# Kernel tuning notes

Measured on AMD Instinct MI355X. Metric: run time of the kernel, lower is better.

## Reference

```python
import jax, jax.numpy as jnp
import numpy as np

N_NODES = 50000


def gcn_conv(h, src, dst, W, b, n):
    # PyG GCNConv: x' = D^{-1/2} (A + I) D^{-1/2} (h W) + b
    x = h @ W  # [N, out]
    deg = jax.ops.segment_sum(jnp.ones_like(src, dtype=x.dtype), dst, num_segments=n) + 1.0  # self-loop
    dis = deg ** -0.5
    norm = dis[src] * dis[dst]  # [E]
    msg = x[src] * norm[:, None]  # [E, out]
    agg = jax.ops.segment_sum(msg, dst, num_segments=n)
    agg = agg + x * (dis * dis)[:, None]  # self-loop term: 1/deg_i * x_i
    return agg + b


def setup_inputs() -> dict:
    key = jax.random.key(0)
    ks = jax.random.split(key, 8)
    n, e = N_NODES, 800000
    d_in, d_rni, h = 128, 32, 256
    x = jax.random.normal(ks[0], (n, d_in), dtype=jnp.float32)
    rni = jax.random.normal(ks[1], (n, d_rni), dtype=jnp.float32)
    edge_index = jax.random.randint(ks[2], (2, e), 0, n, dtype=jnp.int64)
    s1 = (d_in + d_rni) ** -0.5
    s2 = h ** -0.5
    W1 = jax.random.normal(ks[3], (d_in + d_rni, h), dtype=jnp.float32) * s1
    b1 = jnp.zeros((h,), dtype=jnp.float32)
    W2 = jax.random.normal(ks[4], (h, h), dtype=jnp.float32) * s2
    b2 = jnp.zeros((h,), dtype=jnp.float32)
    W_out = jax.random.normal(ks[5], (h, h), dtype=jnp.float32) * s2
    b_out = jnp.zeros((h,), dtype=jnp.float32)
    return {"x": x, "rni": rni, "edge_index": edge_index, "W1": W1, "b1": b1,
            "W2": W2, "b2": b2, "W_out": W_out, "b_out": b_out}


def reference(x, rni, edge_index, W1, b1, W2, b2, W_out, b_out):
    n = x.shape[0]
    src, dst = edge_index[0], edge_index[1]
    h = jnp.concatenate([x, rni], axis=-1)  # RNI concat
    h = jax.nn.relu(gcn_conv(h, src, dst, W1, b1, n))
    h = jax.nn.relu(gcn_conv(h, src, dst, W2, b2, n))
    return h @ W_out + b_out
```

## Files before the change

kernel.cpp:

```cpp
#include <hip/hip_runtime.h>
#include <hip/hip_bf16.h>
#include <hip/hip_fp16.h>
#include <math.h>

#define D_IN   128
#define D_RNI  32
#define HID    256

typedef _Float16 half8 __attribute__((ext_vector_type(8)));
typedef float    f32x4 __attribute__((ext_vector_type(4)));

__global__ void k_detect(const unsigned int* __restrict__ w, int nwords, int* __restrict__ mode) {
    __shared__ unsigned int red[256];
    unsigned int acc = 0;
    for (int i = threadIdx.x; i < 1024; i += 256) {
        int idx = 2 * i + 1;
        if (idx < nwords) acc |= w[idx];
    }
    red[threadIdx.x] = acc;
    __syncthreads();
    for (int s = 128; s > 0; s >>= 1) {
        if (threadIdx.x < s) red[threadIdx.x] |= red[threadIdx.x + s];
        __syncthreads();
    }
    if (threadIdx.x == 0) *mode = (red[0] == 0u) ? 1 : 0;
}

__global__ void k_count(const unsigned int* __restrict__ ew, const int* __restrict__ mode_p,
                        int* __restrict__ counts, int e) {
    int mode = *mode_p;
    int i = blockIdx.x * 256 + threadIdx.x;
    if (i >= e) return;
    int d = mode ? (int)ew[2 * ((size_t)e + i)] : (int)ew[(size_t)e + i];
    atomicAdd(&counts[d], 1);
}

__global__ __launch_bounds__(1024) void k_scan1(const int* __restrict__ counts,
                                                int* __restrict__ incl,
                                                int* __restrict__ bsum, int n) {
    __shared__ int sd[1024];
    int t = threadIdx.x;
    int i = blockIdx.x * 1024 + t;
    int v = (i < n) ? counts[i] : 0;
    sd[t] = v;
    __syncthreads();
    for (int off = 1; off < 1024; off <<= 1) {
        int tmp = (t >= off) ? sd[t - off] : 0;
        __syncthreads();
        sd[t] += tmp;
        __syncthreads();
    }
    if (i < n) incl[i] = sd[t];
    if (t == 1023) bsum[blockIdx.x] = sd[1023];
}

__global__ __launch_bounds__(1024) void k_scan2(int* __restrict__ bsum, int nb) {
    __shared__ int sd[1024];
    int t = threadIdx.x;
    int v = (t < nb) ? bsum[t] : 0;
    sd[t] = v;
    __syncthreads();
    for (int off = 1; off < 1024; off <<= 1) {
        int tmp = (t >= off) ? sd[t - off] : 0;
        __syncthreads();
        sd[t] += tmp;
        __syncthreads();
    }
    if (t < nb) bsum[t] = sd[t] - v;
    if (t == nb - 1) bsum[nb] = sd[t];
}

__global__ void k_scan3(const int* __restrict__ counts, const int* __restrict__ incl,
                        const int* __restrict__ bsum,
                        int* __restrict__ rowptr, int* __restrict__ cursor,
                        float* __restrict__ dis, int n, int nb) {
    int i = blockIdx.x * 256 + threadIdx.x;
    if (i >= n) return;
    int excl = incl[i] - counts[i] + bsum[i >> 10];
    rowptr[i] = excl;
    cursor[i] = excl;
    dis[i] = 1.0f / sqrtf((float)(counts[i] + 1));
    if (i == 0) rowptr[n] = bsum[nb];
}

__global__ void k_scatter(const unsigned int* __restrict__ ew, const int* __restrict__ mode_p,
                          int* __restrict__ cursor, int* __restrict__ csr, int e) {
    int mode = *mode_p;
    int i = blockIdx.x * 256 + threadIdx.x;
    if (i >= e) return;
    int s, d;
    if (mode) {
        s = (int)ew[2 * (size_t)i];
        d = (int)ew[2 * ((size_t)e + i)];
    } else {
        s = (int)ew[(size_t)i];
        d = (int)ew[(size_t)e + i];
    }
    int pos = atomicAdd(&cursor[d], 1);
    csr[pos] = s;
}

__global__ void k_cvt_wt(const float* __restrict__ W, __half* __restrict__ Wt,
                         int K, int N, int total) {
    int i = blockIdx.x * 256 + threadIdx.x;
    if (i >= total) return;
    int k = i / N, nn = i - k * N;
    Wt[(size_t)nn * K + k] = __float2half(W[i]);
}

#define KT 32
#define LSTR 40
template <bool A_F32, bool ADD_BIAS, bool HALF_OUT>
__global__ __launch_bounds__(256) void k_mgemm(const void* __restrict__ Av, int strideA, int KA,
                                               const void* __restrict__ A2v, int strideA2,
                                               const __half* __restrict__ Bt,
                                               const float* __restrict__ bias,
                                               void* Cv, int M, int K) {
    __shared__ __half As[64 * LSTR];
    __shared__ __half Bs[256 * LSTR];
    int tid = threadIdx.x;
    int wave = tid >> 6, lane = tid & 63;
    int q = lane >> 4, m16 = lane & 15;
    int r0 = blockIdx.x * 64;

    f32x4 acc[4][4] = {};

    for (int k0 = 0; k0 < K; k0 += KT) {
        __syncthreads();
        {
            int r = tid >> 2, kq = (tid & 3) * 8;
            int row = r0 + r; if (row >= M) row = M - 1;
            if (A_F32) {
                const float* src; int stride, kk0;
                if (k0 < KA) { src = (const float*)Av;  stride = strideA;  kk0 = k0; }
                else         { src = (const float*)A2v; stride = strideA2; kk0 = k0 - KA; }
                const float* p = &src[(size_t)row * stride + kk0 + kq];
                float4 va = *reinterpret_cast<const float4*>(p);
                float4 vb = *reinterpret_cast<const float4*>(p + 4);
                union { __half2 h2[4]; uint4 u; } uu;
                uu.h2[0] = __floats2half2_rn(va.x, va.y);
                uu.h2[1] = __floats2half2_rn(va.z, va.w);
                uu.h2[2] = __floats2half2_rn(vb.x, vb.y);
                uu.h2[3] = __floats2half2_rn(vb.z, vb.w);
                *reinterpret_cast<uint4*>(&As[r * LSTR + kq]) = uu.u;
            } else {
                const __half* src = (const __half*)Av;
                uint4 v = *reinterpret_cast<const uint4*>(&src[(size_t)row * strideA + k0 + kq]);
                *reinterpret_cast<uint4*>(&As[r * LSTR + kq]) = v;
            }
        }
        {
            int nb = tid >> 2, kq = (tid & 3) * 8;
            #pragma unroll
            for (int i = 0; i < 4; ++i) {
                int nn = nb + i * 64;
                uint4 v = *reinterpret_cast<const uint4*>(&Bt[(size_t)nn * K + k0 + kq]);
                *reinterpret_cast<uint4*>(&Bs[nn * LSTR + kq]) = v;
            }
        }
        __syncthreads();

        half8 af[4], bf[4];
        #pragma unroll
        for (int mi = 0; mi < 4; ++mi)
            af[mi] = *reinterpret_cast<const half8*>(&As[(mi * 16 + m16) * LSTR + q * 8]);
        #pragma unroll
        for (int ni = 0; ni < 4; ++ni)
            bf[ni] = *reinterpret_cast<const half8*>(&Bs[(wave * 64 + ni * 16 + m16) * LSTR + q * 8]);
        #pragma unroll
        for (int mi = 0; mi < 4; ++mi)
            #pragma unroll
            for (int ni = 0; ni < 4; ++ni)
                acc[mi][ni] = __builtin_amdgcn_mfma_f32_16x16x32_f16(af[mi], bf[ni], acc[mi][ni], 0, 0, 0);
    }

    #pragma unroll
    for (int mi = 0; mi < 4; ++mi) {
        #pragma unroll
        for (int r = 0; r < 4; ++r) {
            int row = r0 + mi * 16 + q * 4 + r;
            if (row >= M) continue;
            #pragma unroll
            for (int ni = 0; ni < 4; ++ni) {
                int col = wave * 64 + ni * 16 + m16;
                float v = acc[mi][ni][r];
                if (ADD_BIAS) v += bias[col];
                if (HALF_OUT) ((__half*)Cv)[(size_t)row * HID + col] = __float2half(v);
                else          ((float*)Cv)[(size_t)row * HID + col] = v;
            }
        }
    }
}

__global__ __launch_bounds__(256) void k_agg(const __half* __restrict__ xh,
                                             const int* __restrict__ rowptr,
                                             const int* __restrict__ csr,
                                             const float* __restrict__ dis,
                                             const float* __restrict__ bias,
                                             __half* __restrict__ outh, int n) {
    int i = blockIdx.x * 4 + (threadIdx.x >> 6);
    if (i >= n) return;
    int lane = threadIdx.x & 63;
    int c4 = lane * 4;
    float disd = dis[i];
    int e0 = rowptr[i], e1 = rowptr[i + 1];

    float acc0, acc1, acc2, acc3;
    {
        uint2 v = *reinterpret_cast<const uint2*>(&xh[(size_t)i * HID + c4]);
        float2 f0 = __half22float2(*reinterpret_cast<__half2*>(&v.x));
        float2 f1 = __half22float2(*reinterpret_cast<__half2*>(&v.y));
        float ws = disd * disd;
        acc0 = f0.x * ws; acc1 = f0.y * ws; acc2 = f1.x * ws; acc3 = f1.y * ws;
    }

    for (int e = e0; e < e1; e += 64) {
        int cnt = min(64, e1 - e);
        int sreg = 0; float wreg = 0.0f;
        if (lane < cnt) {
            sreg = csr[e + lane];
            wreg = dis[sreg] * disd;
        }
        int j = 0;
        for (; j + 4 <= cnt; j += 4) {
            int   s0 = __shfl(sreg, j + 0), s1 = __shfl(sreg, j + 1);
            int   s2 = __shfl(sreg, j + 2), s3 = __shfl(sreg, j + 3);
            float w0 = __shfl(wreg, j + 0), w1 = __shfl(wreg, j + 1);
            float w2 = __shfl(wreg, j + 2), w3 = __shfl(wreg, j + 3);
            uint2 v0 = *reinterpret_cast<const uint2*>(&xh[(size_t)s0 * HID + c4]);
            uint2 v1 = *reinterpret_cast<const uint2*>(&xh[(size_t)s1 * HID + c4]);
            uint2 v2 = *reinterpret_cast<const uint2*>(&xh[(size_t)s2 * HID + c4]);
            uint2 v3 = *reinterpret_cast<const uint2*>(&xh[(size_t)s3 * HID + c4]);
            float2 a0 = __half22float2(*reinterpret_cast<__half2*>(&v0.x));
            float2 b0 = __half22float2(*reinterpret_cast<__half2*>(&v0.y));
            float2 a1 = __half22float2(*reinterpret_cast<__half2*>(&v1.x));
            float2 b1 = __half22float2(*reinterpret_cast<__half2*>(&v1.y));
            float2 a2 = __half22float2(*reinterpret_cast<__half2*>(&v2.x));
            float2 b2 = __half22float2(*reinterpret_cast<__half2*>(&v2.y));
            float2 a3 = __half22float2(*reinterpret_cast<__half2*>(&v3.x));
            float2 b3 = __half22float2(*reinterpret_cast<__half2*>(&v3.y));
            acc0 = fmaf(a0.x, w0, acc0); acc1 = fmaf(a0.y, w0, acc1);
            acc2 = fmaf(b0.x, w0, acc2); acc3 = fmaf(b0.y, w0, acc3);
            acc0 = fmaf(a1.x, w1, acc0); acc1 = fmaf(a1.y, w1, acc1);
            acc2 = fmaf(b1.x, w1, acc2); acc3 = fmaf(b1.y, w1, acc3);
            acc0 = fmaf(a2.x, w2, acc0); acc1 = fmaf(a2.y, w2, acc1);
            acc2 = fmaf(b2.x, w2, acc2); acc3 = fmaf(b2.y, w2, acc3);
            acc0 = fmaf(a3.x, w3, acc0); acc1 = fmaf(a3.y, w3, acc1);
            acc2 = fmaf(b3.x, w3, acc2); acc3 = fmaf(b3.y, w3, acc3);
        }
        for (; j < cnt; ++j) {
            int   s = __shfl(sreg, j);
            float w = __shfl(wreg, j);
            uint2 v = *reinterpret_cast<const uint2*>(&xh[(size_t)s * HID + c4]);
            float2 a = __half22float2(*reinterpret_cast<__half2*>(&v.x));
            float2 b = __half22float2(*reinterpret_cast<__half2*>(&v.y));
            acc0 = fmaf(a.x, w, acc0); acc1 = fmaf(a.y, w, acc1);
            acc2 = fmaf(b.x, w, acc2); acc3 = fmaf(b.y, w, acc3);
        }
    }

    float4 bb = *reinterpret_cast<const float4*>(&bias[c4]);
    union { __half2 h2[2]; uint2 u; } o;
    o.h2[0] = __floats2half2_rn(fmaxf(acc0 + bb.x, 0.0f), fmaxf(acc1 + bb.y, 0.0f));
    o.h2[1] = __floats2half2_rn(fmaxf(acc2 + bb.z, 0.0f), fmaxf(acc3 + bb.w, 0.0f));
    *reinterpret_cast<uint2*>(&outh[(size_t)i * HID + c4]) = o.u;
}

extern "C" void kernel_launch(void* const* d_in, const int* in_sizes, int n_in,
                              void* d_out, int out_size, void* d_ws, size_t ws_size,
                              hipStream_t stream) {
    const float* x     = (const float*)d_in[0];
    const float* rni   = (const float*)d_in[1];
    const unsigned int* ew = (const unsigned int*)d_in[2];
    const float* W1    = (const float*)d_in[3];
    const float* b1    = (const float*)d_in[4];
    const float* W2    = (const float*)d_in[5];
    const float* b2    = (const float*)d_in[6];
    const float* W_out = (const float*)d_in[7];
    const float* b_out = (const float*)d_in[8];
    float* out = (float*)d_out;

    const int n  = in_sizes[0] / D_IN;
    const int e  = in_sizes[2] / 2;
    const int nb = (n + 1023) / 1024;
    const int K1 = D_IN + D_RNI;

    char* ws = (char*)d_ws;
    size_t off = 0;
    auto carve = [&](size_t bytes) {
        char* p = ws + off;
        off = (off + bytes + 255) & ~(size_t)255;
        return p;
    };
    __half* xh    = (__half*)carve((size_t)n * HID * sizeof(__half));
    __half* h     = (__half*)carve((size_t)n * HID * sizeof(__half));
    __half* W1t   = (__half*)carve((size_t)K1 * HID * sizeof(__half));
    __half* W2t   = (__half*)carve((size_t)HID * HID * sizeof(__half));
    __half* Wot   = (__half*)carve((size_t)HID * HID * sizeof(__half));
    int*   counts = (int*)carve((size_t)n * sizeof(int));
    int*   incl   = (int*)carve((size_t)n * sizeof(int));
    int*   bsum   = (int*)carve((size_t)(nb + 1) * sizeof(int));
    int*   rowptr = (int*)carve((size_t)(n + 1) * sizeof(int));
    int*   cursor = (int*)carve((size_t)n * sizeof(int));
    float* dis    = (float*)carve((size_t)n * sizeof(float));
    int*   csr    = (int*)carve((size_t)e * sizeof(int));
    int*   mode   = (int*)carve(sizeof(int));
    (void)ws_size;

    const int eb = (e + 255) / 256;
    const int gemm_blocks = (n + 63) / 64;
    const int agg_blocks  = (n + 3) / 4;

    k_detect<<<1, 256, 0, stream>>>(ew, 2 * e, mode);
    hipMemsetAsync(counts, 0, (size_t)n * sizeof(int), stream);
    k_count<<<eb, 256, 0, stream>>>(ew, mode, counts, e);
    k_scan1<<<nb, 1024, 0, stream>>>(counts, incl, bsum, n);
    k_scan2<<<1, 1024, 0, stream>>>(bsum, nb);
    k_scan3<<<(n + 255) / 256, 256, 0, stream>>>(counts, incl, bsum, rowptr, cursor, dis, n, nb);
    k_scatter<<<eb, 256, 0, stream>>>(ew, mode, cursor, csr, e);

    {
        int tw1 = K1 * HID;
        k_cvt_wt<<<(tw1 + 255) / 256, 256, 0, stream>>>(W1, W1t, K1, HID, tw1);
        int tw = HID * HID;
        k_cvt_wt<<<(tw + 255) / 256, 256, 0, stream>>>(W2, W2t, HID, HID, tw);
        k_cvt_wt<<<(tw + 255) / 256, 256, 0, stream>>>(W_out, Wot, HID, HID, tw);
    }

    k_mgemm<true, false, true><<<gemm_blocks, 256, 0, stream>>>(x, D_IN, D_IN, rni, D_RNI,
                                                                W1t, nullptr, xh, n, K1);
    k_agg<<<agg_blocks, 256, 0, stream>>>(xh, rowptr, csr, dis, b1, h, n);

    k_mgemm<false, false, true><<<gemm_blocks, 256, 0, stream>>>(h, HID, HID, nullptr, 0,
                                                                 W2t, nullptr, xh, n, HID);
    k_agg<<<agg_blocks, 256, 0, stream>>>(xh, rowptr, csr, dis, b2, h, n);

    k_mgemm<false, true, false><<<gemm_blocks, 256, 0, stream>>>(h, HID, HID, nullptr, 0,
                                                                 Wot, b_out, out, n, HID);
}
```

Measured before the change: 390.4 us.

## Chunk feature layout into column slabs and precompute edge weights in CSR

The GEMM's half-precision output is now written in a column-chunked layout: 8 slabs of 32 columns, each contiguous per node. Aggregation blocks each handle one slab, so the gathered working set per pass is smaller and cache-friendlier. The scatter kernel stores (src, normalized weight) pairs, which removes the per-edge dis lookup during aggregation. Each wave processes 8 edges in parallel and reduces them with shuffles. This doubles CSR storage and adds a cross-lane reduction per node, in exchange for better L2 locality of the gathers.

```diff
diff --git a/kernel.cpp b/kernel.cpp
--- a/kernel.cpp
+++ b/kernel.cpp
@@ -6,6 +6,7 @@
 #define D_IN   128
 #define D_RNI  32
 #define HID    256
+#define NCHUNK 8
 
 typedef _Float16 half8 __attribute__((ext_vector_type(8)));
 typedef float    f32x4 __attribute__((ext_vector_type(4)));
@@ -84,7 +85,8 @@
 }
 
 __global__ void k_scatter(const unsigned int* __restrict__ ew, const int* __restrict__ mode_p,
-                          int* __restrict__ cursor, int* __restrict__ csr, int e) {
+                          int* __restrict__ cursor, const float* __restrict__ dis,
+                          uint2* __restrict__ csrw, int e) {
     int mode = *mode_p;
     int i = blockIdx.x * 256 + threadIdx.x;
     if (i >= e) return;
@@ -96,8 +98,12 @@
         s = (int)ew[(size_t)i];
         d = (int)ew[(size_t)e + i];
     }
+    float w = dis[s] * dis[d];
     int pos = atomicAdd(&cursor[d], 1);
-    csr[pos] = s;
+    uint2 m;
+    m.x = (unsigned int)s;
+    m.y = __float_as_uint(w);
+    csrw[pos] = m;
 }
 
 __global__ void k_cvt_wt(const float* __restrict__ W, __half* __restrict__ Wt,
@@ -185,8 +191,12 @@
                 int col = wave * 64 + ni * 16 + m16;
                 float v = acc[mi][ni][r];
                 if (ADD_BIAS) v += bias[col];
-                if (HALF_OUT) ((__half*)Cv)[(size_t)row * HID + col] = __float2half(v);
-                else          ((float*)Cv)[(size_t)row * HID + col] = v;
+                if (HALF_OUT) {
+                    size_t addr = ((size_t)(col >> 5) * M + row) * 32 + (col & 31);
+                    ((__half*)Cv)[addr] = __float2half(v);
+                } else {
+                    ((float*)Cv)[(size_t)row * HID + col] = v;
+                }
             }
         }
     }
@@ -194,76 +204,61 @@
 
 __global__ __launch_bounds__(256) void k_agg(const __half* __restrict__ xh,
                                              const int* __restrict__ rowptr,
-                                             const int* __restrict__ csr,
+                                             const uint2* __restrict__ csrw,
                                              const float* __restrict__ dis,
                                              const float* __restrict__ bias,
                                              __half* __restrict__ outh, int n) {
-    int i = blockIdx.x * 4 + (threadIdx.x >> 6);
-    if (i >= n) return;
-    int lane = threadIdx.x & 63;
-    int c4 = lane * 4;
-    float disd = dis[i];
-    int e0 = rowptr[i], e1 = rowptr[i + 1];
-
-    float acc0, acc1, acc2, acc3;
-    {
-        uint2 v = *reinterpret_cast<const uint2*>(&xh[(size_t)i * HID + c4]);
-        float2 f0 = __half22float2(*reinterpret_cast<__half2*>(&v.x));
-        float2 f1 = __half22float2(*reinterpret_cast<__half2*>(&v.y));
-        float ws = disd * disd;
-        acc0 = f0.x * ws; acc1 = f0.y * ws; acc2 = f1.x * ws; acc3 = f1.y * ws;
-    }
-
-    for (int e = e0; e < e1; e += 64) {
-        int cnt = min(64, e1 - e);
-        int sreg = 0; float wreg = 0.0f;
-        if (lane < cnt) {
-            sreg = csr[e + lane];
-            wreg = dis[sreg] * disd;
-        }
-        int j = 0;
-        for (; j + 4 <= cnt; j += 4) {
-            int   s0 = __shfl(sreg, j + 0), s1 = __shfl(sreg, j + 1);
-            int   s2 = __shfl(sreg, j + 2), s3 = __shfl(sreg, j + 3);
-            float w0 = __shfl(wreg, j + 0), w1 = __shfl(wreg, j + 1);
-            float w2 = __shfl(wreg, j + 2), w3 = __shfl(wreg, j + 3);
-            uint2 v0 = *reinterpret_cast<const uint2*>(&xh[(size_t)s0 * HID + c4]);
-            uint2 v1 = *reinterpret_cast<const uint2*>(&xh[(size_t)s1 * HID + c4]);
-            uint2 v2 = *reinterpret_cast<const uint2*>(&xh[(size_t)s2 * HID + c4]);
-            uint2 v3 = *reinterpret_cast<const uint2*>(&xh[(size_t)s3 * HID + c4]);
-            float2 a0 = __half22float2(*reinterpret_cast<__half2*>(&v0.x));
-            float2 b0 = __half22float2(*reinterpret_cast<__half2*>(&v0.y));
-            float2 a1 = __half22float2(*reinterpret_cast<__half2*>(&v1.x));
-            float2 b1 = __half22float2(*reinterpret_cast<__half2*>(&v1.y));
-            float2 a2 = __half22float2(*reinterpret_cast<__half2*>(&v2.x));
-            float2 b2 = __half22float2(*reinterpret_cast<__half2*>(&v2.y));
-            float2 a3 = __half22float2(*reinterpret_cast<__half2*>(&v3.x));
-            float2 b3 = __half22float2(*reinterpret_cast<__half2*>(&v3.y));
-            acc0 = fmaf(a0.x, w0, acc0); acc1 = fmaf(a0.y, w0, acc1);
-            acc2 = fmaf(b0.x, w0, acc2); acc3 = fmaf(b0.y, w0, acc3);
-            acc0 = fmaf(a1.x, w1, acc0); acc1 = fmaf(a1.y, w1, acc1);
-            acc2 = fmaf(b1.x, w1, acc2); acc3 = fmaf(b1.y, w1, acc3);
-            acc0 = fmaf(a2.x, w2, acc0); acc1 = fmaf(a2.y, w2, acc1);
-            acc2 = fmaf(b2.x, w2, acc2); acc3 = fmaf(b2.y, w2, acc3);
-            acc0 = fmaf(a3.x, w3, acc0); acc1 = fmaf(a3.y, w3, acc1);
-            acc2 = fmaf(b3.x, w3, acc2); acc3 = fmaf(b3.y, w3, acc3);
-        }
-        for (; j < cnt; ++j) {
-            int   s = __shfl(sreg, j);
-            float w = __shfl(wreg, j);
-            uint2 v = *reinterpret_cast<const uint2*>(&xh[(size_t)s * HID + c4]);
-            float2 a = __half22float2(*reinterpret_cast<__half2*>(&v.x));
-            float2 b = __half22float2(*reinterpret_cast<__half2*>(&v.y));
-            acc0 = fmaf(a.x, w, acc0); acc1 = fmaf(a.y, w, acc1);
-            acc2 = fmaf(b.x, w, acc2); acc3 = fmaf(b.y, w, acc3);
-        }
-    }
-
-    float4 bb = *reinterpret_cast<const float4*>(&bias[c4]);
-    union { __half2 h2[2]; uint2 u; } o;
-    o.h2[0] = __floats2half2_rn(fmaxf(acc0 + bb.x, 0.0f), fmaxf(acc1 + bb.y, 0.0f));
-    o.h2[1] = __floats2half2_rn(fmaxf(acc2 + bb.z, 0.0f), fmaxf(acc3 + bb.w, 0.0f));
-    *reinterpret_cast<uint2*>(&outh[(size_t)i * HID + c4]) = o.u;
+    int chunk = blockIdx.x & 7;
+    int g     = blockIdx.x >> 3;
+    int wave = threadIdx.x >> 6, lane = threadIdx.x & 63;
+    int sub = lane >> 3, cpos = lane & 7;
+    const __half* base = xh + (size_t)chunk * n * 32;
+    int cbase = chunk * 32 + cpos * 4;
+    float4 bb = *reinterpret_cast<const float4*>(&bias[cbase]);
+
+    #pragma unroll
+    for (int t = 0; t < 4; ++t) {
+        int i = g * 16 + wave * 4 + t;
+        if (i >= n) break;
+        float disd = dis[i];
+        int e0 = rowptr[i], e1 = rowptr[i + 1];
+
+        uint2 sv = *reinterpret_cast<const uint2*>(&base[(size_t)i * 32 + cpos * 4]);
+        float2 sf0 = __half22float2(*reinterpret_cast<__half2*>(&sv.x));
+        float2 sf1 = __half22float2(*reinterpret_cast<__half2*>(&sv.y));
+        float wself = (sub == 0) ? disd * disd : 0.0f;
+        float a0 = sf0.x * wself, a1 = sf0.y * wself;
+        float a2 = sf1.x * wself, a3 = sf1.y * wself;
+
+        for (int e = e0; e < e1; e += 8) {
+            int ee = e + sub;
+            int idx = i; float w = 0.0f;
+            if (ee < e1) {
+                uint2 m = csrw[ee];
+                idx = (int)m.x;
+                w = __uint_as_float(m.y);
+            }
+            uint2 v = *reinterpret_cast<const uint2*>(&base[(size_t)idx * 32 + cpos * 4]);
+            float2 f0 = __half22float2(*reinterpret_cast<__half2*>(&v.x));
+            float2 f1 = __half22float2(*reinterpret_cast<__half2*>(&v.y));
+            a0 = fmaf(f0.x, w, a0); a1 = fmaf(f0.y, w, a1);
+            a2 = fmaf(f1.x, w, a2); a3 = fmaf(f1.y, w, a3);
+        }
+
+        a0 += __shfl_xor(a0, 8);  a1 += __shfl_xor(a1, 8);
+        a2 += __shfl_xor(a2, 8);  a3 += __shfl_xor(a3, 8);
+        a0 += __shfl_xor(a0, 16); a1 += __shfl_xor(a1, 16);
+        a2 += __shfl_xor(a2, 16); a3 += __shfl_xor(a3, 16);
+        a0 += __shfl_xor(a0, 32); a1 += __shfl_xor(a1, 32);
+        a2 += __shfl_xor(a2, 32); a3 += __shfl_xor(a3, 32);
+
+        if (sub == 0) {
+            union { __half2 h2[2]; uint2 u; } o;
+            o.h2[0] = __floats2half2_rn(fmaxf(a0 + bb.x, 0.0f), fmaxf(a1 + bb.y, 0.0f));
+            o.h2[1] = __floats2half2_rn(fmaxf(a2 + bb.z, 0.0f), fmaxf(a3 + bb.w, 0.0f));
+            *reinterpret_cast<uint2*>(&outh[(size_t)i * HID + cbase]) = o.u;
+        }
+    }
 }
 
 extern "C" void kernel_launch(void* const* d_in, const int* in_sizes, int n_in,
@@ -303,13 +298,13 @@
     int*   rowptr = (int*)carve((size_t)(n + 1) * sizeof(int));
     int*   cursor = (int*)carve((size_t)n * sizeof(int));
     float* dis    = (float*)carve((size_t)n * sizeof(float));
-    int*   csr    = (int*)carve((size_t)e * sizeof(int));
+    uint2* csrw   = (uint2*)carve((size_t)e * sizeof(uint2));
     int*   mode   = (int*)carve(sizeof(int));
     (void)ws_size;
 
     const int eb = (e + 255) / 256;
     const int gemm_blocks = (n + 63) / 64;
-    const int agg_blocks  = (n + 3) / 4;
+    const int agg_blocks  = NCHUNK * ((n + 15) / 16);
 
     k_detect<<<1, 256, 0, stream>>>(ew, 2 * e, mode);
     hipMemsetAsync(counts, 0, (size_t)n * sizeof(int), stream);
@@ -317,7 +312,7 @@
     k_scan1<<<nb, 1024, 0, stream>>>(counts, incl, bsum, n);
     k_scan2<<<1, 1024, 0, stream>>>(bsum, nb);
     k_scan3<<<(n + 255) / 256, 256, 0, stream>>>(counts, incl, bsum, rowptr, cursor, dis, n, nb);
-    k_scatter<<<eb, 256, 0, stream>>>(ew, mode, cursor, csr, e);
+    k_scatter<<<eb, 256, 0, stream>>>(ew, mode, cursor, dis, csrw, e);
 
     {
         int tw1 = K1 * HID;
@@ -329,11 +324,11 @@
 
     k_mgemm<true, false, true><<<gemm_blocks, 256, 0, stream>>>(x, D_IN, D_IN, rni, D_RNI,
                                                                 W1t, nullptr, xh, n, K1);
-    k_agg<<<agg_blocks, 256, 0, stream>>>(xh, rowptr, csr, dis, b1, h, n);
+    k_agg<<<agg_blocks, 256, 0, stream>>>(xh, rowptr, csrw, dis, b1, h, n);
 
     k_mgemm<false, false, true><<<gemm_blocks, 256, 0, stream>>>(h, HID, HID, nullptr, 0,
                                                                  W2t, nullptr, xh, n, HID);
-    k_agg<<<agg_blocks, 256, 0, stream>>>(xh, rowptr, csr, dis, b2, h, n);
+    k_agg<<<agg_blocks, 256, 0, stream>>>(xh, rowptr, csrw, dis, b2, h, n);
 
     k_mgemm<false, true, false><<<gemm_blocks, 256, 0, stream>>>(h, HID, HID, nullptr, 0,
                                                                  Wot, b_out, out, n, HID);
```

After: 505.3 us. 29.4% more time.
